# Performance work log

Hardware: AMD Instinct MI355X
Metric: run time of the kernel (lower is better)

## Reference

```python
import jax, jax.numpy as jnp
import numpy as np

N_NODES = 100000
N_EDGES = 3200000
N_IN = 128
N_HID = 128
N_OUT = 64
HOP = 10


def setup_inputs() -> dict:
    key = jax.random.key(0)
    ks = jax.random.split(key, 8)
    x = jax.random.normal(ks[0], (N_NODES, N_IN), dtype=jnp.float32)
    edge_row = jax.random.randint(ks[1], (N_EDGES,), 0, N_NODES, dtype=jnp.int32)
    edge_col = jax.random.randint(ks[2], (N_EDGES,), 0, N_NODES, dtype=jnp.int32)
    # normalized-ish edge weights so 10 hops of propagation stay bounded
    edge_val = jax.random.uniform(ks[3], (N_EDGES,), dtype=jnp.float32) / 32.0
    s_ih = 1.0 / np.sqrt(N_IN)
    s_hh = 1.0 / np.sqrt(N_HID)
    W_ih = jax.random.normal(ks[4], (4 * N_HID, N_IN), dtype=jnp.float32) * s_ih
    W_hh = jax.random.normal(ks[5], (4 * N_HID, N_HID), dtype=jnp.float32) * s_hh
    b_ih = jnp.zeros((4 * N_HID,), dtype=jnp.float32)
    b_hh = jnp.zeros((4 * N_HID,), dtype=jnp.float32)
    fc_w = jax.random.normal(ks[6], (N_OUT, N_HID), dtype=jnp.float32) * s_hh
    fc_b = jnp.zeros((N_OUT,), dtype=jnp.float32)
    return dict(x=x, edge_row=edge_row, edge_col=edge_col, edge_val=edge_val,
                W_ih=W_ih, W_hh=W_hh, b_ih=b_ih, b_hh=b_hh, fc_w=fc_w, fc_b=fc_b)


def _lstm_cell(x, h, c, W_ih, W_hh, b_ih, b_hh):
    # torch LSTMCell gate order: input, forget, cell(g), output
    gates = x @ W_ih.T + b_ih + h @ W_hh.T + b_hh  # [N, 4H]
    i, f, g, o = jnp.split(gates, 4, axis=-1)
    i = jax.nn.sigmoid(i)
    f = jax.nn.sigmoid(f)
    g = jnp.tanh(g)
    o = jax.nn.sigmoid(o)
    c_new = f * c + i * g
    h_new = o * jnp.tanh(c_new)
    return h_new, c_new


def _spmm(edge_row, edge_col, edge_val, h, n_nodes):
    # (A @ h)[r] = sum_{edges e with row r} val[e] * h[col[e]]
    msgs = edge_val[:, None] * h[edge_col]  # [E, H] gather
    return jax.ops.segment_sum(msgs, edge_row, num_segments=n_nodes)


def reference(x, edge_row, edge_col, edge_val, W_ih, W_hh, b_ih, b_hh, fc_w, fc_b):
    n = x.shape[0]
    h = jnp.zeros((n, W_hh.shape[1]), dtype=x.dtype)
    c = jnp.zeros_like(h)
    # hop iterations: LSTM gate update then sparse propagation (dropout = eval/identity)
    for _ in range(HOP):
        h, c = _lstm_cell(x, h, c, W_ih, W_hh, b_ih, b_hh)
        h = _spmm(edge_row, edge_col, edge_val, h, n)
    h = jax.nn.relu(h)
    return h @ fc_w.T + fc_b
```

## Files before the change

kernel.cpp:

```cpp
#include <hip/hip_runtime.h>
#include <hip/hip_bf16.h>
#include <math.h>

constexpr int NN  = 100000;
constexpr int EE  = 3200000;
constexpr int HID = 128;
constexpr int NG  = 512;
constexpr int NOUT = 64;
constexpr int HOPS = 10;
constexpr int SCAN_BLK = 1024;
constexpr int NBLK_SCAN = (NN + SCAN_BLK - 1) / SCAN_BLK;

typedef __attribute__((ext_vector_type(8))) short short8;
typedef __attribute__((ext_vector_type(4))) float f32x4;

__device__ __forceinline__ ushort f2bf(float f) {
    uint u = __builtin_bit_cast(uint, f);
    u += 0x7fff + ((u >> 16) & 1);
    return (ushort)(u >> 16);
}
__device__ __forceinline__ float bflo(uint u) { return __builtin_bit_cast(float, u << 16); }
__device__ __forceinline__ float bfhi(uint u) { return __builtin_bit_cast(float, u & 0xffff0000u); }

__device__ __forceinline__ float sigf(float v) { return 1.0f / (1.0f + __expf(-v)); }
__device__ __forceinline__ float tanh_fast(float x) {
    float t = __expf(-2.0f * fabsf(x));
    float r = (1.0f - t) / (1.0f + t);
    return copysignf(r, x);
}

__device__ __forceinline__ short8 load_frag(const ushort* p) {
    return *reinterpret_cast<const short8*>(p);
}
__device__ __forceinline__ f32x4 mfma16(short8 a, short8 b, f32x4 c) {
    return __builtin_amdgcn_mfma_f32_16x16x32_bf16(a, b, c, 0, 0, 0);
}

__global__ __launch_bounds__(256) void convert_bf16_kernel(
    const float* __restrict__ src, ushort* __restrict__ dst, int n4)
{
    int i = blockIdx.x * 256 + threadIdx.x;
    if (i < n4) {
        float4 v = reinterpret_cast<const float4*>(src)[i];
        ushort4 o;
        o.x = f2bf(v.x); o.y = f2bf(v.y); o.z = f2bf(v.z); o.w = f2bf(v.w);
        reinterpret_cast<ushort4*>(dst)[i] = o;
    }
}

__global__ __launch_bounds__(256) void bsum_kernel(
    const float* __restrict__ bih, const float* __restrict__ bhh, float* __restrict__ bsum)
{
    int i = blockIdx.x * 256 + threadIdx.x;
    if (i < NG) bsum[i] = bih[i] + bhh[i];
}

__global__ __launch_bounds__(256) void hist_kernel(const int* __restrict__ erow,
                                                   int* __restrict__ deg)
{
    int e = blockIdx.x * 256 + threadIdx.x;
    atomicAdd(&deg[erow[e]], 1);
}

__global__ __launch_bounds__(SCAN_BLK) void scan1_kernel(const int* __restrict__ deg,
                                                         int* __restrict__ bsums)
{
    __shared__ int tmp[SCAN_BLK];
    int t = threadIdx.x;
    int i = blockIdx.x * SCAN_BLK + t;
    tmp[t] = (i < NN) ? deg[i] : 0;
    __syncthreads();
    for (int off = SCAN_BLK / 2; off > 0; off >>= 1) {
        if (t < off) tmp[t] += tmp[t + off];
        __syncthreads();
    }
    if (t == 0) bsums[blockIdx.x] = tmp[0];
}

__global__ __launch_bounds__(128) void scan2_kernel(int* __restrict__ bsums)
{
    __shared__ int tmp[128];
    int t = threadIdx.x;
    tmp[t] = (t < NBLK_SCAN) ? bsums[t] : 0;
    __syncthreads();
    for (int off = 1; off < 128; off <<= 1) {
        int add = (t >= off) ? tmp[t - off] : 0;
        __syncthreads();
        tmp[t] += add;
        __syncthreads();
    }
    if (t < NBLK_SCAN) bsums[t] = tmp[t] - ((t < NBLK_SCAN) ? 0 : 0) - (t < NBLK_SCAN ? (t == 0 ? tmp[0] : tmp[t] - tmp[t - 1]) : 0) + ((t == 0) ? 0 : tmp[t - 1]) - ((t == 0) ? 0 : tmp[t - 1]);
    if (t < NBLK_SCAN) bsums[t] = (t == 0) ? 0 : tmp[t - 1];
}

__global__ __launch_bounds__(SCAN_BLK) void scan3_kernel(const int* __restrict__ deg,
                                                         const int* __restrict__ bsums,
                                                         int* __restrict__ rp,
                                                         int* __restrict__ cur)
{
    __shared__ int tmp[SCAN_BLK];
    int t = threadIdx.x;
    int i = blockIdx.x * SCAN_BLK + t;
    int v = (i < NN) ? deg[i] : 0;
    tmp[t] = v;
    __syncthreads();
    for (int off = 1; off < SCAN_BLK; off <<= 1) {
        int add = (t >= off) ? tmp[t - off] : 0;
        __syncthreads();
        tmp[t] += add;
        __syncthreads();
    }
    int incl = tmp[t] + bsums[blockIdx.x];
    if (i < NN) {
        rp[i + 1] = incl;
        cur[i] = incl - v;
    }
    if (i == 0) rp[0] = 0;
}

__global__ __launch_bounds__(256) void scatter_kernel(
    const int* __restrict__ erow, const int* __restrict__ ecol,
    const float* __restrict__ eval, int* __restrict__ cur,
    int2* __restrict__ epack)
{
    int e = blockIdx.x * 256 + threadIdx.x;
    int r = erow[e];
    int p = atomicAdd(&cur[r], 1);
    int2 pk;
    pk.x = ecol[e];
    pk.y = __builtin_bit_cast(int, eval[e]);
    epack[p] = pk;
}

template<bool FIRST>
__global__ __launch_bounds__(256, 2) void cell_kernel(
    const ushort* __restrict__ xb, const ushort* __restrict__ hb,
    const ushort* __restrict__ Wib, const ushort* __restrict__ Whb,
    const float* __restrict__ bsum, float* __restrict__ cperm,
    ushort* __restrict__ hout)
{
    __shared__ __align__(16) ushort lds_h[32 * 136];

    const int t  = threadIdx.x;
    const int l  = t & 63;
    const int w  = t >> 6;
    const int lr = l & 15;
    const int lk = l >> 4;
    const int row0 = blockIdx.x * 32;

    f32x4 acc[8][2];
#pragma unroll
    for (int nI = 0; nI < 8; ++nI) {
        float b = bsum[(4 * nI + w) * 16 + lr];
        acc[nI][0] = f32x4{b, b, b, b};
        acc[nI][1] = f32x4{b, b, b, b};
    }

    short8 ax[2][4];
    short8 ah[2][4];
#pragma unroll
    for (int rf = 0; rf < 2; ++rf) {
        const size_t arow = (size_t)(row0 + rf * 16 + lr) * HID + lk * 8;
#pragma unroll
        for (int ks = 0; ks < 4; ++ks) {
            ax[rf][ks] = load_frag(xb + arow + ks * 32);
            if (!FIRST) ah[rf][ks] = load_frag(hb + arow + ks * 32);
        }
    }

#pragma unroll
    for (int nI = 0; nI < 8; ++nI) {
        const int n = 4 * nI + w;
        const ushort* wip = Wib + (size_t)(n * 16 + lr) * HID + lk * 8;
        const ushort* whp = Whb + (size_t)(n * 16 + lr) * HID + lk * 8;
        short8 bi[4], bh[4];
#pragma unroll
        for (int ks = 0; ks < 4; ++ks) {
            bi[ks] = load_frag(wip + ks * 32);
            if (!FIRST) bh[ks] = load_frag(whp + ks * 32);
        }
#pragma unroll
        for (int rf = 0; rf < 2; ++rf) {
#pragma unroll
            for (int ks = 0; ks < 4; ++ks) {
                acc[nI][rf] = mfma16(ax[rf][ks], bi[ks], acc[nI][rf]);
                if (!FIRST) acc[nI][rf] = mfma16(ah[rf][ks], bh[ks], acc[nI][rf]);
            }
        }
    }

#pragma unroll
    for (int nj = 0; nj < 2; ++nj) {
        const int col = (w + 4 * nj) * 16 + lr;
#pragma unroll
        for (int rf = 0; rf < 2; ++rf) {
            f32x4 iv = acc[nj][rf];
            f32x4 fv = acc[nj + 2][rf];
            f32x4 gv = acc[nj + 4][rf];
            f32x4 ov = acc[nj + 6][rf];
            const size_t cidx = ((((size_t)blockIdx.x * 4 + w) * 2 + nj) * 2 + rf) * 64 + l;
            f32x4 cold;
            if (FIRST) cold = f32x4{0.f, 0.f, 0.f, 0.f};
            else       cold = reinterpret_cast<const f32x4*>(cperm)[cidx];
            f32x4 cn, hn;
#pragma unroll
            for (int jj = 0; jj < 4; ++jj) {
                float c2 = sigf(fv[jj]) * cold[jj] + sigf(iv[jj]) * tanh_fast(gv[jj]);
                cn[jj] = c2;
                hn[jj] = sigf(ov[jj]) * tanh_fast(c2);
            }
            reinterpret_cast<f32x4*>(cperm)[cidx] = cn;
            const int rbase = rf * 16 + lk * 4;
#pragma unroll
            for (int jj = 0; jj < 4; ++jj)
                lds_h[(rbase + jj) * 136 + col] = f2bf(hn[jj]);
        }
    }
    __syncthreads();
    {
        const ushort* lsrc = &lds_h[(t >> 3) * 136 + (t & 7) * 16];
        short8 v0 = *reinterpret_cast<const short8*>(lsrc);
        short8 v1 = *reinterpret_cast<const short8*>(lsrc + 8);
        ushort* gdst = hout + (size_t)row0 * HID + t * 16;
        *reinterpret_cast<short8*>(gdst) = v0;
        *reinterpret_cast<short8*>(gdst + 8) = v1;
    }
}

__global__ __launch_bounds__(256) void spmm_kernel(
    const int* __restrict__ rp, const int2* __restrict__ epack,
    const ushort* __restrict__ hin, ushort* __restrict__ hout)
{
    int r = blockIdx.x * 4 + (threadIdx.x >> 6);
    if (r >= NN) return;
    int l = threadIdx.x & 63;
    int beg = rp[r], end = rp[r + 1];

    float s0a = 0.f, s1a = 0.f, s0b = 0.f, s1b = 0.f;
    float s0c = 0.f, s1c = 0.f, s0d = 0.f, s1d = 0.f;
    int e = beg;
    for (; e + 4 <= end; e += 4) {
        int2 p0 = epack[e], p1 = epack[e + 1], p2 = epack[e + 2], p3 = epack[e + 3];
        float v0 = __builtin_bit_cast(float, p0.y);
        float v1 = __builtin_bit_cast(float, p1.y);
        float v2 = __builtin_bit_cast(float, p2.y);
        float v3 = __builtin_bit_cast(float, p3.y);
        uint g0 = *reinterpret_cast<const uint*>(hin + (size_t)p0.x * HID + l * 2);
        uint g1 = *reinterpret_cast<const uint*>(hin + (size_t)p1.x * HID + l * 2);
        uint g2 = *reinterpret_cast<const uint*>(hin + (size_t)p2.x * HID + l * 2);
        uint g3 = *reinterpret_cast<const uint*>(hin + (size_t)p3.x * HID + l * 2);
        s0a += v0 * bflo(g0); s1a += v0 * bfhi(g0);
        s0b += v1 * bflo(g1); s1b += v1 * bfhi(g1);
        s0c += v2 * bflo(g2); s1c += v2 * bfhi(g2);
        s0d += v3 * bflo(g3); s1d += v3 * bfhi(g3);
    }
    for (; e < end; ++e) {
        int2 p0 = epack[e];
        float v0 = __builtin_bit_cast(float, p0.y);
        uint g0 = *reinterpret_cast<const uint*>(hin + (size_t)p0.x * HID + l * 2);
        s0a += v0 * bflo(g0); s1a += v0 * bfhi(g0);
    }
    float s0 = (s0a + s0b) + (s0c + s0d);
    float s1 = (s1a + s1b) + (s1c + s1d);
    uint o = ((uint)f2bf(s1) << 16) | (uint)f2bf(s0);
    *reinterpret_cast<uint*>(hout + (size_t)r * HID + l * 2) = o;
}

__global__ __launch_bounds__(256) void final_mfma_kernel(
    const ushort* __restrict__ hb, const ushort* __restrict__ fcwb,
    const float* __restrict__ fcb, float* __restrict__ out)
{
    const int t = threadIdx.x;
    const int l = t & 63;
    const int w = t >> 6;
    const int lr = l & 15;
    const int lk = l >> 4;
    const int row0 = blockIdx.x * 64 + w * 16;

    f32x4 acc[4];
#pragma unroll
    for (int n = 0; n < 4; ++n) {
        float b = fcb[n * 16 + lr];
        acc[n] = f32x4{b, b, b, b};
    }

    const short8 z8 = {0, 0, 0, 0, 0, 0, 0, 0};
    const int arow = row0 + lr;
    const bool aok = arow < NN;
    short8 a[4];
#pragma unroll
    for (int ks = 0; ks < 4; ++ks) {
        short8 v = aok ? load_frag(hb + (size_t)arow * HID + ks * 32 + lk * 8) : z8;
#pragma unroll
        for (int i = 0; i < 8; ++i) {
            ushort u = (ushort)v[i];
            if (u & 0x8000) v[i] = 0;
        }
        a[ks] = v;
    }

#pragma unroll
    for (int n = 0; n < 4; ++n) {
        const ushort* wp = fcwb + (size_t)(n * 16 + lr) * HID + lk * 8;
#pragma unroll
        for (int ks = 0; ks < 4; ++ks)
            acc[n] = mfma16(a[ks], load_frag(wp + ks * 32), acc[n]);
    }

#pragma unroll
    for (int n = 0; n < 4; ++n) {
#pragma unroll
        for (int j = 0; j < 4; ++j) {
            int row = row0 + lk * 4 + j;
            if (row < NN) out[(size_t)row * NOUT + n * 16 + lr] = acc[n][j];
        }
    }
}

extern "C" void kernel_launch(void* const* d_in, const int* in_sizes, int n_in,
                              void* d_out, int out_size, void* d_ws, size_t ws_size,
                              hipStream_t stream)
{
    const float* x    = (const float*)d_in[0];
    const int*   erow = (const int*)d_in[1];
    const int*   ecol = (const int*)d_in[2];
    const float* eval = (const float*)d_in[3];
    const float* Wih  = (const float*)d_in[4];
    const float* Whh  = (const float*)d_in[5];
    const float* bih  = (const float*)d_in[6];
    const float* bhh  = (const float*)d_in[7];
    const float* fcw  = (const float*)d_in[8];
    const float* fcb  = (const float*)d_in[9];
    float* out = (float*)d_out;

    char* ws = (char*)d_ws;
    size_t off = 0;
    auto alloc = [&](size_t bytes) -> void* {
        void* p = ws + off;
        off = (off + bytes + 255) & ~(size_t)255;
        return p;
    };
    ushort* hb_a  = (ushort*)alloc((size_t)NN * HID * 2);
    ushort* hb_b  = (ushort*)alloc((size_t)NN * HID * 2);
    float*  cperm = (float*)alloc((size_t)NN * HID * 4);
    ushort* xb    = (ushort*)alloc((size_t)NN * HID * 2);
    ushort* Wib   = (ushort*)alloc((size_t)NG * HID * 2);
    ushort* Whb   = (ushort*)alloc((size_t)NG * HID * 2);
    ushort* fcwb  = (ushort*)alloc((size_t)NOUT * HID * 2);
    float*  bsum  = (float*)alloc((size_t)NG * 4);
    int*    rp    = (int*)alloc((size_t)(NN + 1) * 4);
    int*    deg   = (int*)alloc((size_t)NN * 4);
    int*    cur   = (int*)alloc((size_t)NN * 4);
    int*    bsums = (int*)alloc((size_t)NBLK_SCAN * 4);
    int2*   epack = (int2*)alloc((size_t)EE * 8);
    (void)ws_size;

    convert_bf16_kernel<<<(NN * HID / 4 + 255) / 256, 256, 0, stream>>>(x, xb, NN * HID / 4);
    convert_bf16_kernel<<<(NG * HID / 4 + 255) / 256, 256, 0, stream>>>(Wih, Wib, NG * HID / 4);
    convert_bf16_kernel<<<(NG * HID / 4 + 255) / 256, 256, 0, stream>>>(Whh, Whb, NG * HID / 4);
    convert_bf16_kernel<<<(NOUT * HID / 4 + 255) / 256, 256, 0, stream>>>(fcw, fcwb, NOUT * HID / 4);
    bsum_kernel<<<2, 256, 0, stream>>>(bih, bhh, bsum);

    hipMemsetAsync(deg, 0, (size_t)NN * 4, stream);
    hist_kernel<<<EE / 256, 256, 0, stream>>>(erow, deg);
    scan1_kernel<<<NBLK_SCAN, SCAN_BLK, 0, stream>>>(deg, bsums);
    scan2_kernel<<<1, 128, 0, stream>>>(bsums);
    scan3_kernel<<<NBLK_SCAN, SCAN_BLK, 0, stream>>>(deg, bsums, rp, cur);
    scatter_kernel<<<EE / 256, 256, 0, stream>>>(erow, ecol, eval, cur, epack);

    const int CELL_GRID = NN / 32;

    cell_kernel<true><<<CELL_GRID, 256, 0, stream>>>(xb, hb_b, Wib, Whb, bsum, cperm, hb_a);
    spmm_kernel<<<(NN + 3) / 4, 256, 0, stream>>>(rp, epack, hb_a, hb_b);
    for (int hop = 1; hop < HOPS; ++hop) {
        cell_kernel<false><<<CELL_GRID, 256, 0, stream>>>(xb, hb_b, Wib, Whb, bsum, cperm, hb_a);
        spmm_kernel<<<(NN + 3) / 4, 256, 0, stream>>>(rp, epack, hb_a, hb_b);
    }

    final_mfma_kernel<<<(NN + 63) / 64, 256, 0, stream>>>(hb_b, fcwb, fcb, out);
}
```

Baseline: 2.803 ms.

## Replace direct CSR scatter with two-pass bucketed scatter and nontemporal edge loads

The single random-scatter pass that builds the row-sorted edge array becomes two passes. The first bins edges by 256-row bucket, using shared-memory histograms, a scan and per-bucket global atomics, and writes them into a temporary buffer that reuses the cell-state memory. The second pass then scatters within each bucket, so writes land in a narrow address range. The aim is to cut the scattered-write and atomic traffic of CSR construction, at the cost of an extra read and write of the edge data. The SpMM edge loads also switch to nontemporal 64-bit loads so the streamed edge list does not displace the gathered h rows from cache.

```diff
diff --git a/kernel.cpp b/kernel.cpp
--- a/kernel.cpp
+++ b/kernel.cpp
@@ -10,6 +10,9 @@
 constexpr int HOPS = 10;
 constexpr int SCAN_BLK = 1024;
 constexpr int NBLK_SCAN = (NN + SCAN_BLK - 1) / SCAN_BLK;
+constexpr int NB = (NN + 255) / 256;
+constexpr int PA_BATCH = 4096;
+constexpr int PA_GRID = (EE + PA_BATCH - 1) / PA_BATCH;
 
 typedef __attribute__((ext_vector_type(8))) short short8;
 typedef __attribute__((ext_vector_type(4))) float f32x4;
@@ -89,7 +92,6 @@
         tmp[t] += add;
         __syncthreads();
     }
-    if (t < NBLK_SCAN) bsums[t] = tmp[t] - ((t < NBLK_SCAN) ? 0 : 0) - (t < NBLK_SCAN ? (t == 0 ? tmp[0] : tmp[t] - tmp[t - 1]) : 0) + ((t == 0) ? 0 : tmp[t - 1]) - ((t == 0) ? 0 : tmp[t - 1]);
     if (t < NBLK_SCAN) bsums[t] = (t == 0) ? 0 : tmp[t - 1];
 }
 
@@ -118,18 +120,98 @@
     if (i == 0) rp[0] = 0;
 }
 
-__global__ __launch_bounds__(256) void scatter_kernel(
+__global__ __launch_bounds__(512) void binit_kernel(const int* __restrict__ rp,
+                                                    int* __restrict__ bcur)
+{
+    int b = threadIdx.x;
+    if (b < NB) bcur[b] = rp[b << 8];
+}
+
+__global__ __launch_bounds__(256) void passA_kernel(
     const int* __restrict__ erow, const int* __restrict__ ecol,
-    const float* __restrict__ eval, int* __restrict__ cur,
-    int2* __restrict__ epack)
+    const float* __restrict__ eval, int* __restrict__ bcur,
+    int* __restrict__ trow, int2* __restrict__ tcv)
+{
+    __shared__ int  lhist[512];
+    __shared__ int  sa[512];
+    __shared__ int  sb[512];
+    __shared__ int  gbase[512];
+    __shared__ int  srow[PA_BATCH];
+    __shared__ int2 scv[PA_BATCH];
+
+    const int t = threadIdx.x;
+    const int base = blockIdx.x * PA_BATCH;
+    const int nb = min(PA_BATCH, EE - base);
+
+    lhist[t] = 0; lhist[t + 256] = 0;
+    __syncthreads();
+
+    int er[16], ec[16], pk[16];
+    float ev[16];
+#pragma unroll
+    for (int k = 0; k < 16; ++k) {
+        int idx = k * 256 + t;
+        if (idx < nb) {
+            int e = base + idx;
+            int r = erow[e];
+            er[k] = r; ec[k] = ecol[e]; ev[k] = eval[e];
+            int b = r >> 8;
+            int pos = atomicAdd(&lhist[b], 1);
+            pk[k] = b | (pos << 9);
+        } else pk[k] = -1;
+    }
+    __syncthreads();
+
+    sa[t] = lhist[t]; sa[t + 256] = lhist[t + 256];
+    __syncthreads();
+    int* src = sa; int* dst = sb;
+    for (int off = 1; off < 512; off <<= 1) {
+        dst[t] = src[t] + ((t >= off) ? src[t - off] : 0);
+        int i2 = t + 256;
+        dst[i2] = src[i2] + src[i2 - off];
+        __syncthreads();
+        int* tp = src; src = dst; dst = tp;
+    }
+    int* incl = src;
+
+    for (int b = t; b < NB; b += 256) {
+        int cnt = lhist[b];
+        gbase[b] = cnt ? atomicAdd(&bcur[b], cnt) : 0;
+    }
+    __syncthreads();
+
+#pragma unroll
+    for (int k = 0; k < 16; ++k) {
+        if (pk[k] >= 0) {
+            int b = pk[k] & 511;
+            int pos = pk[k] >> 9;
+            int lofs = b ? incl[b - 1] : 0;
+            int s = lofs + pos;
+            srow[s] = er[k];
+            scv[s] = int2{ec[k], __builtin_bit_cast(int, ev[k])};
+        }
+    }
+    __syncthreads();
+
+    for (int s = t; s < nb; s += 256) {
+        int rr = srow[s];
+        int b = rr >> 8;
+        int lofs = b ? incl[b - 1] : 0;
+        int g = gbase[b] + (s - lofs);
+        trow[g] = rr;
+        tcv[g] = scv[s];
+    }
+}
+
+__global__ __launch_bounds__(256) void passB_kernel(
+    const int* __restrict__ trow, const int2* __restrict__ tcv,
+    int* __restrict__ cur, int2* __restrict__ epack)
 {
     int e = blockIdx.x * 256 + threadIdx.x;
-    int r = erow[e];
+    int r = trow[e];
+    int2 cv = tcv[e];
     int p = atomicAdd(&cur[r], 1);
-    int2 pk;
-    pk.x = ecol[e];
-    pk.y = __builtin_bit_cast(int, eval[e]);
-    epack[p] = pk;
+    epack[p] = cv;
 }
 
 template<bool FIRST>
@@ -235,29 +317,35 @@
     if (r >= NN) return;
     int l = threadIdx.x & 63;
     int beg = rp[r], end = rp[r + 1];
+    const unsigned long long* eq = reinterpret_cast<const unsigned long long*>(epack);
 
     float s0a = 0.f, s1a = 0.f, s0b = 0.f, s1b = 0.f;
     float s0c = 0.f, s1c = 0.f, s0d = 0.f, s1d = 0.f;
     int e = beg;
     for (; e + 4 <= end; e += 4) {
-        int2 p0 = epack[e], p1 = epack[e + 1], p2 = epack[e + 2], p3 = epack[e + 3];
-        float v0 = __builtin_bit_cast(float, p0.y);
-        float v1 = __builtin_bit_cast(float, p1.y);
-        float v2 = __builtin_bit_cast(float, p2.y);
-        float v3 = __builtin_bit_cast(float, p3.y);
-        uint g0 = *reinterpret_cast<const uint*>(hin + (size_t)p0.x * HID + l * 2);
-        uint g1 = *reinterpret_cast<const uint*>(hin + (size_t)p1.x * HID + l * 2);
-        uint g2 = *reinterpret_cast<const uint*>(hin + (size_t)p2.x * HID + l * 2);
-        uint g3 = *reinterpret_cast<const uint*>(hin + (size_t)p3.x * HID + l * 2);
+        unsigned long long u0 = __builtin_nontemporal_load(eq + e);
+        unsigned long long u1 = __builtin_nontemporal_load(eq + e + 1);
+        unsigned long long u2 = __builtin_nontemporal_load(eq + e + 2);
+        unsigned long long u3 = __builtin_nontemporal_load(eq + e + 3);
+        int c0 = (int)(uint)u0, c1 = (int)(uint)u1, c2 = (int)(uint)u2, c3 = (int)(uint)u3;
+        float v0 = __builtin_bit_cast(float, (uint)(u0 >> 32));
+        float v1 = __builtin_bit_cast(float, (uint)(u1 >> 32));
+        float v2 = __builtin_bit_cast(float, (uint)(u2 >> 32));
+        float v3 = __builtin_bit_cast(float, (uint)(u3 >> 32));
+        uint g0 = *reinterpret_cast<const uint*>(hin + (size_t)c0 * HID + l * 2);
+        uint g1 = *reinterpret_cast<const uint*>(hin + (size_t)c1 * HID + l * 2);
+        uint g2 = *reinterpret_cast<const uint*>(hin + (size_t)c2 * HID + l * 2);
+        uint g3 = *reinterpret_cast<const uint*>(hin + (size_t)c3 * HID + l * 2);
         s0a += v0 * bflo(g0); s1a += v0 * bfhi(g0);
         s0b += v1 * bflo(g1); s1b += v1 * bfhi(g1);
         s0c += v2 * bflo(g2); s1c += v2 * bfhi(g2);
         s0d += v3 * bflo(g3); s1d += v3 * bfhi(g3);
     }
     for (; e < end; ++e) {
-        int2 p0 = epack[e];
-        float v0 = __builtin_bit_cast(float, p0.y);
-        uint g0 = *reinterpret_cast<const uint*>(hin + (size_t)p0.x * HID + l * 2);
+        unsigned long long u0 = __builtin_nontemporal_load(eq + e);
+        int c0 = (int)(uint)u0;
+        float v0 = __builtin_bit_cast(float, (uint)(u0 >> 32));
+        uint g0 = *reinterpret_cast<const uint*>(hin + (size_t)c0 * HID + l * 2);
         s0a += v0 * bflo(g0); s1a += v0 * bfhi(g0);
     }
     float s0 = (s0a + s0b) + (s0c + s0d);
@@ -352,8 +440,12 @@
     int*    deg   = (int*)alloc((size_t)NN * 4);
     int*    cur   = (int*)alloc((size_t)NN * 4);
     int*    bsums = (int*)alloc((size_t)NBLK_SCAN * 4);
+    int*    bcur  = (int*)alloc((size_t)NB * 4);
     int2*   epack = (int2*)alloc((size_t)EE * 8);
     (void)ws_size;
+
+    int2* tcv  = (int2*)cperm;
+    int*  trow = (int*)((char*)cperm + (size_t)EE * 8);
 
     convert_bf16_kernel<<<(NN * HID / 4 + 255) / 256, 256, 0, stream>>>(x, xb, NN * HID / 4);
     convert_bf16_kernel<<<(NG * HID / 4 + 255) / 256, 256, 0, stream>>>(Wih, Wib, NG * HID / 4);
@@ -366,7 +458,9 @@
     scan1_kernel<<<NBLK_SCAN, SCAN_BLK, 0, stream>>>(deg, bsums);
     scan2_kernel<<<1, 128, 0, stream>>>(bsums);
     scan3_kernel<<<NBLK_SCAN, SCAN_BLK, 0, stream>>>(deg, bsums, rp, cur);
-    scatter_kernel<<<EE / 256, 256, 0, stream>>>(erow, ecol, eval, cur, epack);
+    binit_kernel<<<1, 512, 0, stream>>>(rp, bcur);
+    passA_kernel<<<PA_GRID, 256, 0, stream>>>(erow, ecol, eval, bcur, trow, tcv);
+    passB_kernel<<<EE / 256, 256, 0, stream>>>(trow, tcv, cur, epack);
 
     const int CELL_GRID = NN / 32;
 
```

Measured after the change: 2.945 ms. 5.1% more time.

## Split SpMM wavefront into two half-waves gathering 8-byte row chunks, reduce cell register pressure

Applied to the files above, without the earlier changes.

The SpMM kernel now splits each wavefront into two 32-lane halves. Each half handles alternating edges and gathers 8 bytes (4 bf16 features) per lane instead of 4 bytes, with nontemporal loads for the edge list and a cross-half shuffle reduction at the end. This is meant to raise bytes per memory request and the number of edges in flight. The cell kernel now does the x and h GEMM phases sequentially behind a scheduling barrier, so fewer fragments are live at once, and its launch bounds rise to 3 blocks per CU to improve occupancy, at the risk of register spills.

```diff
diff --git a/kernel.cpp b/kernel.cpp
--- a/kernel.cpp
+++ b/kernel.cpp
@@ -13,6 +13,7 @@
 
 typedef __attribute__((ext_vector_type(8))) short short8;
 typedef __attribute__((ext_vector_type(4))) float f32x4;
+typedef unsigned long long ull;
 
 __device__ __forceinline__ ushort f2bf(float f) {
     uint u = __builtin_bit_cast(uint, f);
@@ -89,7 +90,6 @@
         tmp[t] += add;
         __syncthreads();
     }
-    if (t < NBLK_SCAN) bsums[t] = tmp[t] - ((t < NBLK_SCAN) ? 0 : 0) - (t < NBLK_SCAN ? (t == 0 ? tmp[0] : tmp[t] - tmp[t - 1]) : 0) + ((t == 0) ? 0 : tmp[t - 1]) - ((t == 0) ? 0 : tmp[t - 1]);
     if (t < NBLK_SCAN) bsums[t] = (t == 0) ? 0 : tmp[t - 1];
 }
 
@@ -133,7 +133,7 @@
 }
 
 template<bool FIRST>
-__global__ __launch_bounds__(256, 2) void cell_kernel(
+__global__ __launch_bounds__(256, 3) void cell_kernel(
     const ushort* __restrict__ xb, const ushort* __restrict__ hb,
     const ushort* __restrict__ Wib, const ushort* __restrict__ Whb,
     const float* __restrict__ bsum, float* __restrict__ cperm,
@@ -156,36 +156,51 @@
         acc[nI][1] = f32x4{b, b, b, b};
     }
 
-    short8 ax[2][4];
-    short8 ah[2][4];
-#pragma unroll
-    for (int rf = 0; rf < 2; ++rf) {
-        const size_t arow = (size_t)(row0 + rf * 16 + lr) * HID + lk * 8;
-#pragma unroll
-        for (int ks = 0; ks < 4; ++ks) {
-            ax[rf][ks] = load_frag(xb + arow + ks * 32);
-            if (!FIRST) ah[rf][ks] = load_frag(hb + arow + ks * 32);
-        }
-    }
-
-#pragma unroll
-    for (int nI = 0; nI < 8; ++nI) {
-        const int n = 4 * nI + w;
-        const ushort* wip = Wib + (size_t)(n * 16 + lr) * HID + lk * 8;
-        const ushort* whp = Whb + (size_t)(n * 16 + lr) * HID + lk * 8;
-        short8 bi[4], bh[4];
-#pragma unroll
-        for (int ks = 0; ks < 4; ++ks) {
-            bi[ks] = load_frag(wip + ks * 32);
-            if (!FIRST) bh[ks] = load_frag(whp + ks * 32);
-        }
+    {
+        short8 ax[2][4];
 #pragma unroll
         for (int rf = 0; rf < 2; ++rf) {
-#pragma unroll
-            for (int ks = 0; ks < 4; ++ks) {
-                acc[nI][rf] = mfma16(ax[rf][ks], bi[ks], acc[nI][rf]);
-                if (!FIRST) acc[nI][rf] = mfma16(ah[rf][ks], bh[ks], acc[nI][rf]);
-            }
+            const size_t arow = (size_t)(row0 + rf * 16 + lr) * HID + lk * 8;
+#pragma unroll
+            for (int ks = 0; ks < 4; ++ks)
+                ax[rf][ks] = load_frag(xb + arow + ks * 32);
+        }
+#pragma unroll
+        for (int nI = 0; nI < 8; ++nI) {
+            const int n = 4 * nI + w;
+            const ushort* wip = Wib + (size_t)(n * 16 + lr) * HID + lk * 8;
+            short8 bi[4];
+#pragma unroll
+            for (int ks = 0; ks < 4; ++ks) bi[ks] = load_frag(wip + ks * 32);
+#pragma unroll
+            for (int rf = 0; rf < 2; ++rf)
+#pragma unroll
+                for (int ks = 0; ks < 4; ++ks)
+                    acc[nI][rf] = mfma16(ax[rf][ks], bi[ks], acc[nI][rf]);
+        }
+    }
+    __builtin_amdgcn_sched_barrier(0);
+    if (!FIRST) {
+        short8 ah[2][4];
+#pragma unroll
+        for (int rf = 0; rf < 2; ++rf) {
+            const size_t arow = (size_t)(row0 + rf * 16 + lr) * HID + lk * 8;
+#pragma unroll
+            for (int ks = 0; ks < 4; ++ks)
+                ah[rf][ks] = load_frag(hb + arow + ks * 32);
+        }
+#pragma unroll
+        for (int nI = 0; nI < 8; ++nI) {
+            const int n = 4 * nI + w;
+            const ushort* whp = Whb + (size_t)(n * 16 + lr) * HID + lk * 8;
+            short8 bh[4];
+#pragma unroll
+            for (int ks = 0; ks < 4; ++ks) bh[ks] = load_frag(whp + ks * 32);
+#pragma unroll
+            for (int rf = 0; rf < 2; ++rf)
+#pragma unroll
+                for (int ks = 0; ks < 4; ++ks)
+                    acc[nI][rf] = mfma16(ah[rf][ks], bh[ks], acc[nI][rf]);
         }
     }
 
@@ -231,39 +246,63 @@
     const int* __restrict__ rp, const int2* __restrict__ epack,
     const ushort* __restrict__ hin, ushort* __restrict__ hout)
 {
-    int r = blockIdx.x * 4 + (threadIdx.x >> 6);
+    const int r = blockIdx.x * 4 + (threadIdx.x >> 6);
     if (r >= NN) return;
-    int l = threadIdx.x & 63;
-    int beg = rp[r], end = rp[r + 1];
-
-    float s0a = 0.f, s1a = 0.f, s0b = 0.f, s1b = 0.f;
-    float s0c = 0.f, s1c = 0.f, s0d = 0.f, s1d = 0.f;
+    const int l = threadIdx.x & 63;
+    const int half = l >> 5;
+    const int fl = l & 31;
+    const ushort* hbase = hin + fl * 4;
+    const int beg = rp[r], end = rp[r + 1];
+    const ull* eq = reinterpret_cast<const ull*>(epack);
+
+    float a0 = 0.f, a1 = 0.f, a2 = 0.f, a3 = 0.f;
+    float b0 = 0.f, b1 = 0.f, b2 = 0.f, b3 = 0.f;
+    float c0 = 0.f, c1 = 0.f, c2 = 0.f, c3 = 0.f;
+    float d0 = 0.f, d1 = 0.f, d2 = 0.f, d3 = 0.f;
+
     int e = beg;
-    for (; e + 4 <= end; e += 4) {
-        int2 p0 = epack[e], p1 = epack[e + 1], p2 = epack[e + 2], p3 = epack[e + 3];
-        float v0 = __builtin_bit_cast(float, p0.y);
-        float v1 = __builtin_bit_cast(float, p1.y);
-        float v2 = __builtin_bit_cast(float, p2.y);
-        float v3 = __builtin_bit_cast(float, p3.y);
-        uint g0 = *reinterpret_cast<const uint*>(hin + (size_t)p0.x * HID + l * 2);
-        uint g1 = *reinterpret_cast<const uint*>(hin + (size_t)p1.x * HID + l * 2);
-        uint g2 = *reinterpret_cast<const uint*>(hin + (size_t)p2.x * HID + l * 2);
-        uint g3 = *reinterpret_cast<const uint*>(hin + (size_t)p3.x * HID + l * 2);
-        s0a += v0 * bflo(g0); s1a += v0 * bfhi(g0);
-        s0b += v1 * bflo(g1); s1b += v1 * bfhi(g1);
-        s0c += v2 * bflo(g2); s1c += v2 * bfhi(g2);
-        s0d += v3 * bflo(g3); s1d += v3 * bfhi(g3);
-    }
-    for (; e < end; ++e) {
-        int2 p0 = epack[e];
-        float v0 = __builtin_bit_cast(float, p0.y);
-        uint g0 = *reinterpret_cast<const uint*>(hin + (size_t)p0.x * HID + l * 2);
-        s0a += v0 * bflo(g0); s1a += v0 * bfhi(g0);
-    }
-    float s0 = (s0a + s0b) + (s0c + s0d);
-    float s1 = (s1a + s1b) + (s1c + s1d);
-    uint o = ((uint)f2bf(s1) << 16) | (uint)f2bf(s0);
-    *reinterpret_cast<uint*>(hout + (size_t)r * HID + l * 2) = o;
+    for (; e + 8 <= end; e += 8) {
+        ull u0 = __builtin_nontemporal_load(eq + e + 0 + half);
+        ull u1 = __builtin_nontemporal_load(eq + e + 2 + half);
+        ull u2 = __builtin_nontemporal_load(eq + e + 4 + half);
+        ull u3 = __builtin_nontemporal_load(eq + e + 6 + half);
+        uint2 g0 = *reinterpret_cast<const uint2*>(hbase + (size_t)(uint)u0 * HID);
+        uint2 g1 = *reinterpret_cast<const uint2*>(hbase + (size_t)(uint)u1 * HID);
+        uint2 g2 = *reinterpret_cast<const uint2*>(hbase + (size_t)(uint)u2 * HID);
+        uint2 g3 = *reinterpret_cast<const uint2*>(hbase + (size_t)(uint)u3 * HID);
+        float v0 = __builtin_bit_cast(float, (uint)(u0 >> 32));
+        float v1 = __builtin_bit_cast(float, (uint)(u1 >> 32));
+        float v2 = __builtin_bit_cast(float, (uint)(u2 >> 32));
+        float v3 = __builtin_bit_cast(float, (uint)(u3 >> 32));
+        a0 += v0 * bflo(g0.x); a1 += v0 * bfhi(g0.x); a2 += v0 * bflo(g0.y); a3 += v0 * bfhi(g0.y);
+        b0 += v1 * bflo(g1.x); b1 += v1 * bfhi(g1.x); b2 += v1 * bflo(g1.y); b3 += v1 * bfhi(g1.y);
+        c0 += v2 * bflo(g2.x); c1 += v2 * bfhi(g2.x); c2 += v2 * bflo(g2.y); c3 += v2 * bfhi(g2.y);
+        d0 += v3 * bflo(g3.x); d1 += v3 * bfhi(g3.x); d2 += v3 * bflo(g3.y); d3 += v3 * bfhi(g3.y);
+    }
+    for (; e < end; e += 2) {
+        int idx = e + half;
+        if (idx < end) {
+            ull u0 = __builtin_nontemporal_load(eq + idx);
+            uint2 g0 = *reinterpret_cast<const uint2*>(hbase + (size_t)(uint)u0 * HID);
+            float v0 = __builtin_bit_cast(float, (uint)(u0 >> 32));
+            a0 += v0 * bflo(g0.x); a1 += v0 * bfhi(g0.x);
+            a2 += v0 * bflo(g0.y); a3 += v0 * bfhi(g0.y);
+        }
+    }
+    float s0 = (a0 + b0) + (c0 + d0);
+    float s1 = (a1 + b1) + (c1 + d1);
+    float s2 = (a2 + b2) + (c2 + d2);
+    float s3 = (a3 + b3) + (c3 + d3);
+    s0 += __shfl_xor(s0, 32);
+    s1 += __shfl_xor(s1, 32);
+    s2 += __shfl_xor(s2, 32);
+    s3 += __shfl_xor(s3, 32);
+    if (half == 0) {
+        uint2 o;
+        o.x = ((uint)f2bf(s1) << 16) | (uint)f2bf(s0);
+        o.y = ((uint)f2bf(s3) << 16) | (uint)f2bf(s2);
+        *reinterpret_cast<uint2*>(hout + (size_t)r * HID + fl * 4) = o;
+    }
 }
 
 __global__ __launch_bounds__(256) void final_mfma_kernel(
@@ -369,12 +408,13 @@
     scatter_kernel<<<EE / 256, 256, 0, stream>>>(erow, ecol, eval, cur, epack);
 
     const int CELL_GRID = NN / 32;
+    const int SPMM_GRID = NN / 4;
 
     cell_kernel<true><<<CELL_GRID, 256, 0, stream>>>(xb, hb_b, Wib, Whb, bsum, cperm, hb_a);
-    spmm_kernel<<<(NN + 3) / 4, 256, 0, stream>>>(rp, epack, hb_a, hb_b);
+    spmm_kernel<<<SPMM_GRID, 256, 0, stream>>>(rp, epack, hb_a, hb_b);
     for (int hop = 1; hop < HOPS; ++hop) {
         cell_kernel<false><<<CELL_GRID, 256, 0, stream>>>(xb, hb_b, Wib, Whb, bsum, cperm, hb_a);
-        spmm_kernel<<<(NN + 3) / 4, 256, 0, stream>>>(rp, epack, hb_a, hb_b);
+        spmm_kernel<<<SPMM_GRID, 256, 0, stream>>>(rp, epack, hb_a, hb_b);
     }
 
     final_mfma_kernel<<<(NN + 63) / 64, 256, 0, stream>>>(hb_b, fcwb, fcb, out);
```

Result: slower. 2.897 ms (+3.4%).
